# Kernel optimization log

Measured on AMD Instinct MI355X. Metric: run time of the kernel, lower is better.

## Reference

```python
import jax, jax.numpy as jnp
import numpy as np

STRIDE = (1, 1)
PADDING = (1, 1)
DILATION = (1, 1)


def deform_conv(x, offset, weight, stride=STRIDE, padding=PADDING, dilation=DILATION):
    """Deformable convolution v1 (mmcv layout), deformable_groups=1, groups=1.

    x:      [B, C, H, W]
    offset: [B, 2*kh*kw, Ho, Wo]   pairs ordered (dy, dx) per kernel tap
    weight: [Co, C, kh, kw]
    """
    B, C, H, W = x.shape
    Co, Ci, kh, kw = weight.shape
    sh, sw = stride
    ph, pw = padding
    dh, dw = dilation
    Ho = (H + 2 * ph - (dh * (kh - 1) + 1)) // sh + 1
    Wo = (W + 2 * pw - (dw * (kw - 1) + 1)) // sw + 1
    K2 = kh * kw

    off = offset.reshape(B, K2, 2, Ho, Wo)
    # base sampling grid per kernel tap: [K2, Ho, Wo]
    ky = (jnp.arange(K2) // kw) * dh          # kernel row offsets
    kx = (jnp.arange(K2) % kw) * dw           # kernel col offsets
    hi = jnp.arange(Ho) * sh - ph             # output-row -> input-row base
    wi = jnp.arange(Wo) * sw - pw
    py = off[:, :, 0] + (ky[:, None, None] + hi[None, :, None])  # [B,K2,Ho,Wo]
    px = off[:, :, 1] + (kx[:, None, None] + wi[None, None, :])  # [B,K2,Ho,Wo]

    y0 = jnp.floor(py)
    x0 = jnp.floor(px)
    ly = py - y0
    lx = px - x0
    hy = 1.0 - ly
    hx = 1.0 - lx
    y0i = y0.astype(jnp.int32)
    x0i = x0.astype(jnp.int32)
    y1i = y0i + 1
    x1i = x0i + 1

    xf = x.reshape(B, C, H * W)

    def gather(yi, xi):
        # zero padding outside the image, per-corner validity (DCN semantics)
        valid = (yi >= 0) & (yi < H) & (xi >= 0) & (xi < W)
        yc = jnp.clip(yi, 0, H - 1)
        xc = jnp.clip(xi, 0, W - 1)
        idx = (yc * W + xc).reshape(B, -1)                 # [B, K2*Ho*Wo]
        vals = jax.vmap(lambda xb, ib: xb[:, ib])(xf, idx)  # [B, C, K2*Ho*Wo]
        vals = vals.reshape(B, C, K2, Ho, Wo)
        return vals * valid[:, None].astype(x.dtype)

    # im2col with bilinear sampling: [B, C, K2, Ho, Wo]
    col = (gather(y0i, x0i) * (hy * hx)[:, None]
           + gather(y0i, x1i) * (hy * lx)[:, None]
           + gather(y1i, x0i) * (ly * hx)[:, None]
           + gather(y1i, x1i) * (ly * lx)[:, None])

    # GEMM: out[b,o,h,w] = sum_{c,k} W[o,c,k] * col[b,c,k,h,w]
    out = jnp.einsum('bckhw,ock->bohw', col, weight.reshape(Co, Ci, K2))
    return out


def setup_inputs() -> dict:
    key = jax.random.key(0)
    k1, k2, k3 = jax.random.split(key, 3)
    x = jax.random.normal(k1, (4, 256, 64, 64), dtype=jnp.float32)
    offset = jax.random.normal(k2, (4, 18, 64, 64), dtype=jnp.float32)
    n = 256 * 3 * 3
    stdv = 1.0 / np.sqrt(n)
    weight = jax.random.uniform(k3, (256, 256, 3, 3), dtype=jnp.float32,
                                minval=-stdv, maxval=stdv)
    return {"x": x, "offset": offset, "weight": weight}


def reference(x, offset, weight):
    return deform_conv(x, offset, weight)
```

## Files before the change

kernel.cpp:

```cpp
#include <hip/hip_runtime.h>
#include <hip/hip_bf16.h>
#include <cstddef>

#define B_    4
#define C_    256
#define H_    64
#define W_    64
#define CO_   256
#define K2_   9
#define NSTEP 72

typedef __attribute__((ext_vector_type(8))) short short8;
typedef __attribute__((ext_vector_type(4))) float f32x4;

__device__ __forceinline__ unsigned short f2bf(float f) {
    unsigned u = __builtin_bit_cast(unsigned, f);
    u = (u + 0x7fffu + ((u >> 16) & 1u)) >> 16;
    return (unsigned short)u;
}
__device__ __forceinline__ unsigned pack2bf(float lo, float hi) {
    __hip_bfloat162 h = __float22bfloat162_rn(make_float2(lo, hi));
    unsigned r; __builtin_memcpy(&r, &h, 4);
    return r;
}

__global__ void wpack_kernel(const float* __restrict__ w,
                             unsigned short* __restrict__ wpk) {
    const int idx = blockIdx.x * 256 + threadIdx.x;
    if (idx >= NSTEP * 16 * 64) return;
    const int lane = idx & 63;
    const int mt   = (idx >> 6) & 15;
    const int s    = idx >> 10;
    const int o    = mt * 16 + (lane & 15);
    const int cc   = s / 9;
    const int t    = s - 9 * cc;
    const int c0   = cc * 32 + ((lane >> 4) << 3);
    unsigned short h[8];
#pragma unroll
    for (int e = 0; e < 8; ++e)
        h[e] = f2bf(w[(o * C_ + c0 + e) * K2_ + t]);
    uint4 v;
    v.x = h[0] | ((unsigned)h[1] << 16);
    v.y = h[2] | ((unsigned)h[3] << 16);
    v.z = h[4] | ((unsigned)h[5] << 16);
    v.w = h[6] | ((unsigned)h[7] << 16);
    *reinterpret_cast<uint4*>(&wpk[(size_t)idx * 8]) = v;
}

__device__ __forceinline__ short8 loadA(const unsigned short* __restrict__ wpk,
                                        const float* __restrict__ wraw,
                                        int use_pk, int s, int mt, int lane) {
    if (use_pk) {
        return *reinterpret_cast<const short8*>(
            wpk + (((size_t)(s * 16 + mt) * 64 + lane) << 3));
    } else {
        const int cc = s / 9;
        const int t  = s - 9 * cc;
        const int c0 = cc * 32 + ((lane >> 4) << 3);
        const int o  = mt * 16 + (lane & 15);
        short8 r;
#pragma unroll
        for (int e = 0; e < 8; ++e)
            r[e] = (short)f2bf(wraw[(o * C_ + c0 + e) * K2_ + t]);
        return r;
    }
}

__global__ __launch_bounds__(512, 4)
void dcn_mfma_kernel(const float* __restrict__ x,
                     const float* __restrict__ off,
                     const unsigned short* __restrict__ wpk,
                     const float* __restrict__ wraw,
                     float* __restrict__ out,
                     int use_pk) {
    __shared__ __align__(16) float s_win[32 * 528 + 64];
    __shared__ __align__(16) float s_meta[K2_ * 32 * 4];
    __shared__ int s_base[K2_ * 32];
    __shared__ __align__(16) unsigned short s_colb[2][1024];

    const int tid = threadIdx.x;
    const int bid = blockIdx.x;
    const int xcd  = bid & 7;
    const int slot = bid >> 3;
    const int b    = xcd >> 1;
    const int ho   = ((xcd & 1) << 5) | (slot >> 1);
    const int woh  = slot & 1;
    const int wo0  = woh << 5;

    const char* xb8 = (const char*)x + ((size_t)b << 22);

    if (tid < K2_ * 32) {
        const int t = tid >> 5;
        const int p = tid & 31;
        const int pa = wo0 + p;
        const float dy = off[((b * 18 + 2 * t    ) * 64 + ho) * 64 + pa];
        const float dx = off[((b * 18 + 2 * t + 1) * 64 + ho) * 64 + pa];
        const float py = (float)(ho - 1 + t / 3) + dy;
        const float px = (float)(pa - 1 + t % 3) + dx;
        const float y0f = floorf(py), x0f = floorf(px);
        const float ly = py - y0f, lx = px - x0f;
        const float hy = 1.0f - ly, hx = 1.0f - lx;
        const int y0 = (int)y0f, x0 = (int)x0f;
        const int y1 = y0 + 1,   x1 = x0 + 1;
        const bool vy0 = (y0 >= 0) & (y0 < H_);
        const bool vy1 = (y1 >= 0) & (y1 < H_);
        const bool vx0 = (x0 >= 0) & (x0 < W_);
        const bool vx1 = (x1 >= 0) & (x1 < W_);
        const int yc0 = min(max(y0, 0), H_ - 1);
        const int yc1 = min(max(y1, 0), H_ - 1);
        const int xc0 = min(max(x0, 0), W_ - 1);
        const int xc1 = min(max(x1, 0), W_ - 1);
        float w00 = (vy0 && vx0) ? hy * hx : 0.0f;
        float w01 = (vy0 && vx1) ? hy * lx : 0.0f;
        float w10 = (vy1 && vx0) ? ly * hx : 0.0f;
        float w11 = (vy1 && vx1) ? ly * lx : 0.0f;
        const int dys = yc1 - yc0, dxs = xc1 - xc0;
        if (!dxs) { w00 += w01; w01 = 0.0f; w10 += w11; w11 = 0.0f; }
        if (!dys) { w00 += w10; w10 = 0.0f; w01 += w11; w11 = 0.0f; }
        const int r0 = yc0 - (ho - 5);
        const int j0 = xc0 - (wo0 - 8);
        const bool fast = (r0 >= 0) & (r0 + dys <= 10) & (j0 >= 0) & (j0 + dxs <= 47);
        int enc;
        if (fast)
            enc = (r0 * 48 + j0) << 2;
        else
            enc = (int)(0x80000000u
                        | (unsigned)((((yc0 << 6) + xc0) << 2) | (dys << 1) | dxs));
        float* mp = &s_meta[(t * 32 + p) * 4];
        mp[0] = w00; mp[1] = w01; mp[2] = w10; mp[3] = w11;
        s_base[t * 32 + p] = enc;
    }

    int goffv[9];
#pragma unroll
    for (int v = 0; v < 9; ++v) {
        const int i   = tid + v * 512;
        const int cl  = i / 132;
        const int rem = i - cl * 132;
        const int r   = rem / 12;
        const int q   = rem - r * 12;
        const int y   = ho - 5 + r;
        int gof = (((y << 6) + wo0 - 8) << 2) + (q << 4);
        gof = min(max(gof, 0), 16384 - 16);
        if ((unsigned)y >= 64u) gof = 0;
        goffv[v] = (cl << 14) + gof;
    }
    __syncthreads();

    const int lane = tid & 63;
    const int wave = tid >> 6;
    const int wo   = lane & 31;
    const int kk0  = (wave << 2) | ((lane >> 5) << 1);
    const unsigned swr = ((unsigned)(wo >> 4) << 10)
                       | ((unsigned)((wo & 15) | ((kk0 >> 3) << 4)) << 4)
                       | ((unsigned)(kk0 & 7) << 1);
    const unsigned brd = (unsigned)lane << 4;
    const int mt0 = wave << 1;
    const char* winA = (const char*)s_win + kk0 * 2112;

    f32x4 acc[2][2];
#pragma unroll
    for (int m = 0; m < 2; ++m)
#pragma unroll
        for (int nt = 0; nt < 2; ++nt)
            acc[m][nt] = (f32x4)(0.0f);

#define COLT(t_, buf_) do {                                                    \
        const float* mp_ = (const float*)((const char*)s_meta                  \
                                          + (t_) * 512 + (wo << 4));           \
        const float w0_ = mp_[0], w1_ = mp_[1], w2_ = mp_[2], w3_ = mp_[3];    \
        const int mb_ = s_base[(t_) * 32 + wo];                                \
        float vA_, vB_;                                                        \
        if (__builtin_expect(mb_ >= 0, 1)) {                                   \
            const float* pA_ = (const float*)(winA + mb_);                     \
            const float* pB_ = (const float*)(winA + 2112 + mb_);              \
            vA_ = w0_*pA_[0] + w1_*pA_[1] + w2_*pA_[48] + w3_*pA_[49];         \
            vB_ = w0_*pB_[0] + w1_*pB_[1] + w2_*pB_[48] + w3_*pB_[49];         \
        } else {                                                               \
            const int dxb_ = (mb_ & 1) << 2, dyb_ = (mb_ & 2) << 7;            \
            const int o_ = mb_ & 0x3fffc;                                      \
            const char* plA_ = xcb + ((size_t)kk0 << 14);                      \
            const char* plB_ = plA_ + (1 << 14);                               \
            vA_ = w0_ * *(const float*)(plA_ + o_)                             \
                + w1_ * *(const float*)(plA_ + o_ + dxb_)                      \
                + w2_ * *(const float*)(plA_ + o_ + dyb_)                      \
                + w3_ * *(const float*)(plA_ + o_ + dyb_ + dxb_);              \
            vB_ = w0_ * *(const float*)(plB_ + o_)                             \
                + w1_ * *(const float*)(plB_ + o_ + dxb_)                      \
                + w2_ * *(const float*)(plB_ + o_ + dyb_)                      \
                + w3_ * *(const float*)(plB_ + o_ + dyb_ + dxb_);              \
        }                                                                      \
        *(unsigned*)((char*)s_colb[buf_] + swr) = pack2bf(vA_, vB_);           \
    } while (0)

#define GEMMSTEP(a0_, a1_, buf_) do {                                          \
        const char* cb_ = (const char*)s_colb[buf_];                           \
        short8 b0_ = *(const short8*)(cb_ + brd);                              \
        short8 b1_ = *(const short8*)(cb_ + brd + 1024);                       \
        acc[0][0] = __builtin_amdgcn_mfma_f32_16x16x32_bf16(a0_, b0_, acc[0][0], 0, 0, 0); \
        acc[0][1] = __builtin_amdgcn_mfma_f32_16x16x32_bf16(a0_, b1_, acc[0][1], 0, 0, 0); \
        acc[1][0] = __builtin_amdgcn_mfma_f32_16x16x32_bf16(a1_, b0_, acc[1][0], 0, 0, 0); \
        acc[1][1] = __builtin_amdgcn_mfma_f32_16x16x32_bf16(a1_, b1_, acc[1][1], 0, 0, 0); \
    } while (0)

#define BARLG() do {                                                           \
        asm volatile("s_waitcnt lgkmcnt(0)" ::: "memory");                     \
        __builtin_amdgcn_s_barrier();                                          \
    } while (0)

    short8 a0 = loadA(wpk, wraw, use_pk, 0, mt0, lane);
    short8 a1 = loadA(wpk, wraw, use_pk, 0, mt0 + 1, lane);

    for (int cc = 0; cc < 8; ++cc) {
        const char* xcb = xb8 + ((size_t)cc << 19);
        {
            char* wbase = (char*)s_win + (size_t)tid * 16;
            float4 s0 = *(const float4*)(xcb + goffv[0]);
            float4 s1 = *(const float4*)(xcb + goffv[1]);
            float4 s2 = *(const float4*)(xcb + goffv[2]);
            float4 s3 = *(const float4*)(xcb + goffv[3]);
            *(float4*)(wbase +     0) = s0;
            *(float4*)(wbase +  8192) = s1;
            *(float4*)(wbase + 16384) = s2;
            *(float4*)(wbase + 24576) = s3;
            float4 s4 = *(const float4*)(xcb + goffv[4]);
            float4 s5 = *(const float4*)(xcb + goffv[5]);
            float4 s6 = *(const float4*)(xcb + goffv[6]);
            float4 s7 = *(const float4*)(xcb + goffv[7]);
            *(float4*)(wbase + 32768) = s4;
            *(float4*)(wbase + 40960) = s5;
            *(float4*)(wbase + 49152) = s6;
            *(float4*)(wbase + 57344) = s7;
            if (tid < 128) {
                float4 s8 = *(const float4*)(xcb + goffv[8]);
                *(float4*)(wbase + 65536) = s8;
            }
        }
        __syncthreads();

        COLT(0, 0);
        BARLG();

#pragma unroll
        for (int j = 0; j < 9; ++j) {
            const int sj = cc * 9 + j;
            short8 n0, n1;
            const bool pf = (sj + 1 < NSTEP);
            if (pf) {
                n0 = loadA(wpk, wraw, use_pk, sj + 1, mt0, lane);
                n1 = loadA(wpk, wraw, use_pk, sj + 1, mt0 + 1, lane);
            }
            if (j < 8) COLT(j + 1, (j + 1) & 1);
            GEMMSTEP(a0, a1, j & 1);
            BARLG();
            if (pf) { a0 = n0; a1 = n1; }
        }
    }

#undef COLT
#undef GEMMSTEP
#undef BARLG

#pragma unroll
    for (int m = 0; m < 2; ++m) {
        const int ob = (mt0 + m) * 16 + ((lane >> 4) << 2);
#pragma unroll
        for (int r = 0; r < 4; ++r) {
            float* orow = out + (((size_t)(b * CO_ + ob + r) * 64 + ho) * 64 + wo0);
#pragma unroll
            for (int nt = 0; nt < 2; ++nt)
                orow[(nt << 4) | (lane & 15)] = acc[m][nt][r];
        }
    }
}

extern "C" void kernel_launch(void* const* d_in, const int* in_sizes, int n_in,
                              void* d_out, int out_size, void* d_ws, size_t ws_size,
                              hipStream_t stream) {
    const float* x      = (const float*)d_in[0];
    const float* offset = (const float*)d_in[1];
    const float* weight = (const float*)d_in[2];
    float* out = (float*)d_out;

    const size_t pk_bytes = (size_t)NSTEP * 16 * 64 * 8 * 2;
    const int use_pk = (ws_size >= pk_bytes) ? 1 : 0;
    unsigned short* wpk = (unsigned short*)d_ws;

    if (use_pk) {
        wpack_kernel<<<288, 256, 0, stream>>>(weight, wpk);
    }
    dcn_mfma_kernel<<<512, 512, 0, stream>>>(x, offset, wpk, weight, out, use_pk);
}
```

Before: 71.26 us.

## Batch three taps per barrier and overlap next-window staging with GEMM

Per-tap bilinear weights and encodings now live in registers, packed as bf16 pairs, instead of shared memory. The bf16-column buffers hold three taps each, so one barrier now covers three taps instead of one. Loading the next channel chunk's input window is moved into the last GEMM phase of the current chunk. The aim is to cut barrier count and hide window-load latency. In exchange, the weight A-fragments are no longer prefetched one step ahead, and rounding the bilinear weights to bf16 adds a little approximation error.

```diff
diff --git a/kernel.cpp b/kernel.cpp
--- a/kernel.cpp
+++ b/kernel.cpp
@@ -22,6 +22,12 @@
     __hip_bfloat162 h = __float22bfloat162_rn(make_float2(lo, hi));
     unsigned r; __builtin_memcpy(&r, &h, 4);
     return r;
+}
+__device__ __forceinline__ float bflo(unsigned u) {
+    return __builtin_bit_cast(float, u << 16);
+}
+__device__ __forceinline__ float bfhi(unsigned u) {
+    return __builtin_bit_cast(float, u & 0xffff0000u);
 }
 
 __global__ void wpack_kernel(const float* __restrict__ w,
@@ -74,9 +80,7 @@
                      float* __restrict__ out,
                      int use_pk) {
     __shared__ __align__(16) float s_win[32 * 528 + 64];
-    __shared__ __align__(16) float s_meta[K2_ * 32 * 4];
-    __shared__ int s_base[K2_ * 32];
-    __shared__ __align__(16) unsigned short s_colb[2][1024];
+    __shared__ __align__(16) unsigned short s_colb[2][3][1024];
 
     const int tid = threadIdx.x;
     const int bid = blockIdx.x;
@@ -89,10 +93,22 @@
 
     const char* xb8 = (const char*)x + ((size_t)b << 22);
 
-    if (tid < K2_ * 32) {
-        const int t = tid >> 5;
-        const int p = tid & 31;
-        const int pa = wo0 + p;
+    const int lane = tid & 63;
+    const int wave = tid >> 6;
+    const int wo   = lane & 31;
+    const int kk0  = (wave << 2) | ((lane >> 5) << 1);
+    const unsigned swr = ((unsigned)(wo >> 4) << 10)
+                       | ((unsigned)((wo & 15) | ((kk0 >> 3) << 4)) << 4)
+                       | ((unsigned)(kk0 & 7) << 1);
+    const unsigned brd = (unsigned)lane << 4;
+    const int mt0 = wave << 1;
+    const char* winA = (const char*)s_win + kk0 * 2112;
+
+    unsigned mw01[9], mw23[9];
+    int menc[9];
+#pragma unroll
+    for (int t = 0; t < 9; ++t) {
+        const int pa = wo0 + wo;
         const float dy = off[((b * 18 + 2 * t    ) * 64 + ho) * 64 + pa];
         const float dx = off[((b * 18 + 2 * t + 1) * 64 + ho) * 64 + pa];
         const float py = (float)(ho - 1 + t / 3) + dy;
@@ -126,9 +142,9 @@
         else
             enc = (int)(0x80000000u
                         | (unsigned)((((yc0 << 6) + xc0) << 2) | (dys << 1) | dxs));
-        float* mp = &s_meta[(t * 32 + p) * 4];
-        mp[0] = w00; mp[1] = w01; mp[2] = w10; mp[3] = w11;
-        s_base[t * 32 + p] = enc;
+        mw01[t] = pack2bf(w00, w01);
+        mw23[t] = pack2bf(w10, w11);
+        menc[t] = enc;
     }
 
     int goffv[9];
@@ -145,18 +161,6 @@
         if ((unsigned)y >= 64u) gof = 0;
         goffv[v] = (cl << 14) + gof;
     }
-    __syncthreads();
-
-    const int lane = tid & 63;
-    const int wave = tid >> 6;
-    const int wo   = lane & 31;
-    const int kk0  = (wave << 2) | ((lane >> 5) << 1);
-    const unsigned swr = ((unsigned)(wo >> 4) << 10)
-                       | ((unsigned)((wo & 15) | ((kk0 >> 3) << 4)) << 4)
-                       | ((unsigned)(kk0 & 7) << 1);
-    const unsigned brd = (unsigned)lane << 4;
-    const int mt0 = wave << 1;
-    const char* winA = (const char*)s_win + kk0 * 2112;
 
     f32x4 acc[2][2];
 #pragma unroll
@@ -165,11 +169,35 @@
         for (int nt = 0; nt < 2; ++nt)
             acc[m][nt] = (f32x4)(0.0f);
 
-#define COLT(t_, buf_) do {                                                    \
-        const float* mp_ = (const float*)((const char*)s_meta                  \
-                                          + (t_) * 512 + (wo << 4));           \
-        const float w0_ = mp_[0], w1_ = mp_[1], w2_ = mp_[2], w3_ = mp_[3];    \
-        const int mb_ = s_base[(t_) * 32 + wo];                                \
+#define STAGEW(XCB_) do {                                                      \
+        char* wb_ = (char*)s_win + (size_t)tid * 16;                           \
+        float4 s0_ = *(const float4*)((XCB_) + goffv[0]);                      \
+        float4 s1_ = *(const float4*)((XCB_) + goffv[1]);                      \
+        float4 s2_ = *(const float4*)((XCB_) + goffv[2]);                      \
+        float4 s3_ = *(const float4*)((XCB_) + goffv[3]);                      \
+        *(float4*)(wb_ +     0) = s0_;                                         \
+        *(float4*)(wb_ +  8192) = s1_;                                         \
+        *(float4*)(wb_ + 16384) = s2_;                                         \
+        *(float4*)(wb_ + 24576) = s3_;                                         \
+        float4 s4_ = *(const float4*)((XCB_) + goffv[4]);                      \
+        float4 s5_ = *(const float4*)((XCB_) + goffv[5]);                      \
+        float4 s6_ = *(const float4*)((XCB_) + goffv[6]);                      \
+        float4 s7_ = *(const float4*)((XCB_) + goffv[7]);                      \
+        *(float4*)(wb_ + 32768) = s4_;                                         \
+        *(float4*)(wb_ + 40960) = s5_;                                         \
+        *(float4*)(wb_ + 49152) = s6_;                                         \
+        *(float4*)(wb_ + 57344) = s7_;                                         \
+        if (tid < 128) {                                                       \
+            float4 s8_ = *(const float4*)((XCB_) + goffv[8]);                  \
+            *(float4*)(wb_ + 65536) = s8_;                                     \
+        }                                                                      \
+    } while (0)
+
+#define COLT1(T_, BUFB_, JJ_, XCB_) do {                                       \
+        const unsigned u01_ = mw01[T_], u23_ = mw23[T_];                       \
+        const float w0_ = bflo(u01_), w1_ = bfhi(u01_);                        \
+        const float w2_ = bflo(u23_), w3_ = bfhi(u23_);                        \
+        const int mb_ = menc[T_];                                              \
         float vA_, vB_;                                                        \
         if (__builtin_expect(mb_ >= 0, 1)) {                                   \
             const float* pA_ = (const float*)(winA + mb_);                     \
@@ -179,7 +207,7 @@
         } else {                                                               \
             const int dxb_ = (mb_ & 1) << 2, dyb_ = (mb_ & 2) << 7;            \
             const int o_ = mb_ & 0x3fffc;                                      \
-            const char* plA_ = xcb + ((size_t)kk0 << 14);                      \
+            const char* plA_ = (XCB_) + ((size_t)kk0 << 14);                   \
             const char* plB_ = plA_ + (1 << 14);                               \
             vA_ = w0_ * *(const float*)(plA_ + o_)                             \
                 + w1_ * *(const float*)(plA_ + o_ + dxb_)                      \
@@ -190,17 +218,43 @@
                 + w2_ * *(const float*)(plB_ + o_ + dyb_)                      \
                 + w3_ * *(const float*)(plB_ + o_ + dyb_ + dxb_);              \
         }                                                                      \
-        *(unsigned*)((char*)s_colb[buf_] + swr) = pack2bf(vA_, vB_);           \
-    } while (0)
-
-#define GEMMSTEP(a0_, a1_, buf_) do {                                          \
-        const char* cb_ = (const char*)s_colb[buf_];                           \
-        short8 b0_ = *(const short8*)(cb_ + brd);                              \
-        short8 b1_ = *(const short8*)(cb_ + brd + 1024);                       \
-        acc[0][0] = __builtin_amdgcn_mfma_f32_16x16x32_bf16(a0_, b0_, acc[0][0], 0, 0, 0); \
-        acc[0][1] = __builtin_amdgcn_mfma_f32_16x16x32_bf16(a0_, b1_, acc[0][1], 0, 0, 0); \
-        acc[1][0] = __builtin_amdgcn_mfma_f32_16x16x32_bf16(a1_, b0_, acc[1][0], 0, 0, 0); \
-        acc[1][1] = __builtin_amdgcn_mfma_f32_16x16x32_bf16(a1_, b1_, acc[1][1], 0, 0, 0); \
+        *(unsigned*)((char*)(BUFB_) + (JJ_) * 2048 + swr) = pack2bf(vA_, vB_); \
+    } while (0)
+
+#define COL3(T0_, BUFB_, XCB_) do {                                            \
+        COLT1((T0_),     BUFB_, 0, XCB_);                                      \
+        COLT1((T0_) + 1, BUFB_, 1, XCB_);                                      \
+        COLT1((T0_) + 2, BUFB_, 2, XCB_);                                      \
+    } while (0)
+
+#define MFMA_(A_, B_, C_) __builtin_amdgcn_mfma_f32_16x16x32_bf16(A_, B_, C_, 0, 0, 0)
+
+#define GEMM3(S0_, BUFB_) do {                                                 \
+        const short8 a00_ = loadA(wpk, wraw, use_pk, (S0_),     mt0,     lane);\
+        const short8 a01_ = loadA(wpk, wraw, use_pk, (S0_),     mt0 + 1, lane);\
+        const short8 a10_ = loadA(wpk, wraw, use_pk, (S0_) + 1, mt0,     lane);\
+        const short8 a11_ = loadA(wpk, wraw, use_pk, (S0_) + 1, mt0 + 1, lane);\
+        const short8 a20_ = loadA(wpk, wraw, use_pk, (S0_) + 2, mt0,     lane);\
+        const short8 a21_ = loadA(wpk, wraw, use_pk, (S0_) + 2, mt0 + 1, lane);\
+        const char* cb_ = (const char*)(BUFB_);                                \
+        const short8 b00_ = *(const short8*)(cb_ + brd);                       \
+        const short8 b01_ = *(const short8*)(cb_ + brd + 1024);                \
+        const short8 b10_ = *(const short8*)(cb_ + 2048 + brd);                \
+        const short8 b11_ = *(const short8*)(cb_ + 2048 + brd + 1024);         \
+        const short8 b20_ = *(const short8*)(cb_ + 4096 + brd);                \
+        const short8 b21_ = *(const short8*)(cb_ + 4096 + brd + 1024);         \
+        acc[0][0] = MFMA_(a00_, b00_, acc[0][0]);                              \
+        acc[0][1] = MFMA_(a00_, b01_, acc[0][1]);                              \
+        acc[1][0] = MFMA_(a01_, b00_, acc[1][0]);                              \
+        acc[1][1] = MFMA_(a01_, b01_, acc[1][1]);                              \
+        acc[0][0] = MFMA_(a10_, b10_, acc[0][0]);                              \
+        acc[0][1] = MFMA_(a10_, b11_, acc[0][1]);                              \
+        acc[1][0] = MFMA_(a11_, b10_, acc[1][0]);                              \
+        acc[1][1] = MFMA_(a11_, b11_, acc[1][1]);                              \
+        acc[0][0] = MFMA_(a20_, b20_, acc[0][0]);                              \
+        acc[0][1] = MFMA_(a20_, b21_, acc[0][1]);                              \
+        acc[1][0] = MFMA_(a21_, b20_, acc[1][0]);                              \
+        acc[1][1] = MFMA_(a21_, b21_, acc[1][1]);                              \
     } while (0)
 
 #define BARLG() do {                                                           \
@@ -208,57 +262,46 @@
         __builtin_amdgcn_s_barrier();                                          \
     } while (0)
 
-    short8 a0 = loadA(wpk, wraw, use_pk, 0, mt0, lane);
-    short8 a1 = loadA(wpk, wraw, use_pk, 0, mt0 + 1, lane);
+    {
+        const char* xcb0 = xb8;
+        STAGEW(xcb0);
+        __syncthreads();
+        char* buf0 = (char*)s_colb;
+        COL3(0, buf0, xcb0);
+        BARLG();
+    }
 
     for (int cc = 0; cc < 8; ++cc) {
-        const char* xcb = xb8 + ((size_t)cc << 19);
-        {
-            char* wbase = (char*)s_win + (size_t)tid * 16;
-            float4 s0 = *(const float4*)(xcb + goffv[0]);
-            float4 s1 = *(const float4*)(xcb + goffv[1]);
-            float4 s2 = *(const float4*)(xcb + goffv[2]);
-            float4 s3 = *(const float4*)(xcb + goffv[3]);
-            *(float4*)(wbase +     0) = s0;
-            *(float4*)(wbase +  8192) = s1;
-            *(float4*)(wbase + 16384) = s2;
-            *(float4*)(wbase + 24576) = s3;
-            float4 s4 = *(const float4*)(xcb + goffv[4]);
-            float4 s5 = *(const float4*)(xcb + goffv[5]);
-            float4 s6 = *(const float4*)(xcb + goffv[6]);
-            float4 s7 = *(const float4*)(xcb + goffv[7]);
-            *(float4*)(wbase + 32768) = s4;
-            *(float4*)(wbase + 40960) = s5;
-            *(float4*)(wbase + 49152) = s6;
-            *(float4*)(wbase + 57344) = s7;
-            if (tid < 128) {
-                float4 s8 = *(const float4*)(xcb + goffv[8]);
-                *(float4*)(wbase + 65536) = s8;
-            }
+        const char* xcb  = xb8 + ((size_t)cc << 19);
+        const char* xcbN = xb8 + ((size_t)(cc + 1) << 19);
+        const int p = cc & 1;
+        char* bufP = (char*)s_colb + p * 6144;
+        char* bufQ = (char*)s_colb + (p ^ 1) * 6144;
+        const int s0 = cc * 9;
+
+        COL3(3, bufQ, xcb);
+        GEMM3(s0, bufP);
+        BARLG();
+
+        COL3(6, bufP, xcb);
+        GEMM3(s0 + 3, bufQ);
+        BARLG();
+
+        if (cc < 7) STAGEW(xcbN);
+        GEMM3(s0 + 6, bufP);
+        BARLG();
+
+        if (cc < 7) {
+            COL3(0, bufQ, xcbN);
+            BARLG();
         }
-        __syncthreads();
-
-        COLT(0, 0);
-        BARLG();
-
-#pragma unroll
-        for (int j = 0; j < 9; ++j) {
-            const int sj = cc * 9 + j;
-            short8 n0, n1;
-            const bool pf = (sj + 1 < NSTEP);
-            if (pf) {
-                n0 = loadA(wpk, wraw, use_pk, sj + 1, mt0, lane);
-                n1 = loadA(wpk, wraw, use_pk, sj + 1, mt0 + 1, lane);
-            }
-            if (j < 8) COLT(j + 1, (j + 1) & 1);
-            GEMMSTEP(a0, a1, j & 1);
-            BARLG();
-            if (pf) { a0 = n0; a1 = n1; }
-        }
-    }
-
-#undef COLT
-#undef GEMMSTEP
+    }
+
+#undef STAGEW
+#undef COLT1
+#undef COL3
+#undef MFMA_
+#undef GEMM3
 #undef BARLG
 
 #pragma unroll
```

Result: slower. 100.6 us (+41.2%).
